# Kernel tuning notes

Measured on AMD Instinct MI355X. Metric: run time of the kernel, lower is better.

## Reference

```python
import jax, jax.numpy as jnp
import numpy as np

N = 4096      # nodes
E = 131072    # edges
C_IN = 128
HID = 128     # d_model of transformer (= embed_dim used in reshape_to_trans)
OUT = 32      # GNN output channels -> transformer seq_len
HEADS = 8
DH = HID // HEADS
FF = 2048     # torch TransformerEncoderLayer default dim_feedforward
EPS = 1e-5


def layer_norm(x, g, b):
    mu = jnp.mean(x, axis=-1, keepdims=True)
    var = jnp.mean(jnp.square(x - mu), axis=-1, keepdims=True)
    return (x - mu) * jax.lax.rsqrt(var + EPS) * g + b


def setup_inputs() -> dict:
    key = jax.random.key(0)
    ks = jax.random.split(key, 24)
    def rn(k, shape, scale=0.05):
        return jax.random.normal(k, shape, dtype=jnp.float32) * scale
    inp = {
        "x": jax.random.normal(ks[0], (N, C_IN), dtype=jnp.float32),
        "edge_index": jax.random.randint(ks[1], (2, E), 0, N, dtype=jnp.int64),
        # GCN layers
        "Wg1": rn(ks[2], (C_IN, HID)), "bg1": jnp.zeros((HID,), jnp.float32),
        "Wg2": rn(ks[3], (HID, HID)),  "bg2": jnp.zeros((HID,), jnp.float32),
        "Wg3": rn(ks[4], (HID, OUT)),  "bg3": jnp.zeros((OUT,), jnp.float32),
        # MHA
        "Wq": rn(ks[5], (HID, HID)), "bq": jnp.zeros((HID,), jnp.float32),
        "Wk": rn(ks[6], (HID, HID)), "bk": jnp.zeros((HID,), jnp.float32),
        "Wv": rn(ks[7], (HID, HID)), "bv": jnp.zeros((HID,), jnp.float32),
        "Wo": rn(ks[8], (HID, HID)), "bo": jnp.zeros((HID,), jnp.float32),
        "ln1_g": jnp.ones((HID,), jnp.float32), "ln1_b": jnp.zeros((HID,), jnp.float32),
        # FFN
        "W1": rn(ks[9], (HID, FF)),  "b1": jnp.zeros((FF,), jnp.float32),
        "W2": rn(ks[10], (FF, HID)), "b2": jnp.zeros((HID,), jnp.float32),
        "ln2_g": jnp.ones((HID,), jnp.float32), "ln2_b": jnp.zeros((HID,), jnp.float32),
    }
    return inp


def reference(x, edge_index, Wg1, bg1, Wg2, bg2, Wg3, bg3,
              Wq, bq, Wk, bk, Wv, bv, Wo, bo, ln1_g, ln1_b,
              W1, b1, W2, b2, ln2_g, ln2_b):
    # ---- GCN normalization (add self-loops, symmetric D^-1/2 (A+I) D^-1/2) ----
    loop = jnp.arange(N, dtype=edge_index.dtype)
    src = jnp.concatenate([edge_index[0], loop])
    dst = jnp.concatenate([edge_index[1], loop])
    deg = jax.ops.segment_sum(jnp.ones((E + N,), jnp.float32), dst, num_segments=N)
    dinv = jnp.where(deg > 0, jax.lax.rsqrt(deg), 0.0)
    norm = (dinv[src] * dinv[dst])[:, None]  # [E+N, 1]

    def gcn(h, W, b):
        m = h @ W                               # [N, d_out]
        agg = jax.ops.segment_sum(m[src] * norm, dst, num_segments=N)
        return agg + b

    h = jax.nn.relu(gcn(x, Wg1, bg1))
    h = jax.nn.relu(gcn(h, Wg2, bg2))
    h = jax.nn.relu(gcn(h, Wg3, bg3))           # [N, OUT]

    # ---- reshape_to_trans: [N, OUT] -> [N, OUT, HID] (repeat along embed dim) ----
    t = jnp.broadcast_to(h[:, :, None], (N, OUT, HID))

    # ---- TransformerEncoderLayer (post-norm, relu FFN, no dropout at eval) ----
    q = (t @ Wq + bq).reshape(N, OUT, HEADS, DH)
    k = (t @ Wk + bk).reshape(N, OUT, HEADS, DH)
    v = (t @ Wv + bv).reshape(N, OUT, HEADS, DH)
    scores = jnp.einsum("bqhd,bkhd->bhqk", q, k) / jnp.sqrt(jnp.float32(DH))
    attn = jax.nn.softmax(scores, axis=-1)
    ctx = jnp.einsum("bhqk,bkhd->bqhd", attn, v).reshape(N, OUT, HID)
    a = ctx @ Wo + bo
    x1 = layer_norm(t + a, ln1_g, ln1_b)
    f = jax.nn.relu(x1 @ W1 + b1) @ W2 + b2
    out = layer_norm(x1 + f, ln2_g, ln2_b)      # [N, OUT, HID]
    return out
```

## Files before the change

### kernel.cpp

```cpp
#include <hip/hip_runtime.h>

#define NN 4096
#define EE 131072
#define FFD 2048

typedef float f32x4 __attribute__((ext_vector_type(4)));
typedef __bf16 bf16x8 __attribute__((ext_vector_type(8)));
typedef unsigned int u32;
typedef u32 u32x4 __attribute__((ext_vector_type(4)));
typedef unsigned short u16;
typedef u16 u16x8 __attribute__((ext_vector_type(8)));

__device__ __forceinline__ u16 f2bf(float f) {
    unsigned u = __builtin_bit_cast(unsigned, f);
    return (u16)((u + 0x7FFFu + ((u >> 16) & 1u)) >> 16);
}
__device__ __forceinline__ float bf2f(u16 h) {
    unsigned u = ((unsigned)h) << 16;
    return __builtin_bit_cast(float, u);
}
__device__ __forceinline__ u32 cvtpk(float lo, float hi) {
    u32 r;
    asm("v_cvt_pk_bf16_f32 %0, %1, %2" : "=v"(r) : "v"(lo), "v"(hi));
    return r;
}

#define GLD16(g, l) __builtin_amdgcn_global_load_lds(                            \
    (const __attribute__((address_space(1))) void*)(g),                          \
    (__attribute__((address_space(3))) void*)(l), 16, 0, 0)

__device__ __forceinline__ int ldedge(const int* ei, int idx, int is64) {
    return is64 ? ei[2 * idx] : ei[idx];
}

__global__ void k_init(const int* __restrict__ ei, int* __restrict__ flag,
                       int* __restrict__ cnt) {
    if (blockIdx.x == 0) {
        if (threadIdx.x < 64) {
            int v = ei[2 * threadIdx.x + 1];
            unsigned long long any = __ballot(v != 0);
            if (threadIdx.x == 0) *flag = (any == 0ULL) ? 1 : 0;
        }
    } else {
        cnt[(blockIdx.x - 1) * 256 + threadIdx.x] = 0;
    }
}

__global__ void k_degi(const int* __restrict__ ei, const int* __restrict__ flag,
                       int* __restrict__ cnt) {
    int e = blockIdx.x * 256 + threadIdx.x;
    if (e >= EE) return;
    atomicAdd(&cnt[ldedge(ei, EE + e, *flag)], 1);
}
__global__ __launch_bounds__(1024) void k_scan(const int* __restrict__ cnt,
        int* __restrict__ rp, int* __restrict__ cur, float* __restrict__ dinv) {
    __shared__ int tsum[1024];
    int t = threadIdx.x;
    int c0 = cnt[t * 4], c1 = cnt[t * 4 + 1], c2 = cnt[t * 4 + 2], c3 = cnt[t * 4 + 3];
    int s = c0 + c1 + c2 + c3;
    tsum[t] = s;
    dinv[t * 4]     = rsqrtf((float)c0 + 1.0f);
    dinv[t * 4 + 1] = rsqrtf((float)c1 + 1.0f);
    dinv[t * 4 + 2] = rsqrtf((float)c2 + 1.0f);
    dinv[t * 4 + 3] = rsqrtf((float)c3 + 1.0f);
    __syncthreads();
    for (int off = 1; off < 1024; off <<= 1) {
        int v = (t >= off) ? tsum[t - off] : 0;
        __syncthreads();
        tsum[t] += v;
        __syncthreads();
    }
    int excl = tsum[t] - s;
    int p0 = excl, p1 = excl + c0, p2 = p1 + c1, p3 = p2 + c2;
    rp[t * 4] = p0; rp[t * 4 + 1] = p1; rp[t * 4 + 2] = p2; rp[t * 4 + 3] = p3;
    cur[t * 4] = p0; cur[t * 4 + 1] = p1; cur[t * 4 + 2] = p2; cur[t * 4 + 3] = p3;
    if (t == 1023) rp[4096] = excl + s;
}

__global__ __launch_bounds__(256) void k_fuse1(const int* __restrict__ ei,
        const int* __restrict__ flag, int* __restrict__ cur, int* __restrict__ es,
        const float* __restrict__ x, const float* __restrict__ Wg1,
        const float* __restrict__ dinv, float* __restrict__ ms,
        const float* __restrict__ W1, const float* __restrict__ W2,
        u16* __restrict__ w1t, u16* __restrict__ w2t,
        const float* __restrict__ Wq, const float* __restrict__ bq,
        const float* __restrict__ Wk, const float* __restrict__ bk,
        const float* __restrict__ Wv, const float* __restrict__ bv,
        const float* __restrict__ Wo, const float* __restrict__ bo,
        float* __restrict__ tc) {
    __shared__ float sm[384];
    int b = blockIdx.x, t = threadIdx.x;
    if (b < 512) {
        int e = b * 256 + t;
        int is64 = *flag;
        int s = ldedge(ei, e, is64), d = ldedge(ei, EE + e, is64);
        int pos = atomicAdd(&cur[d], 1);
        es[pos] = s;
    } else if (b < 2560) {
        int n0 = (b - 512) * 2, r = t >> 7, e = t & 127;
        sm[r * 128 + e] = x[(size_t)(n0 + r) * 128 + e];
        __syncthreads();
        float a = 0.f;
        #pragma unroll 8
        for (int c = 0; c < 128; ++c) a += sm[r * 128 + c] * Wg1[c * 128 + e];
        ms[(size_t)(n0 + r) * 128 + e] = a * dinv[n0 + r];
    } else if (b < 4608) {
        int bb = b - 2560;
        int tg = (bb & 1023) * 256 + t;
        if (bb < 1024) { int f = tg >> 7, c = tg & 127; w1t[tg] = f2bf(W1[c * 2048 + f]); }
        else           { int o = tg >> 11, f = tg & 2047; w2t[tg] = f2bf(W2[f * 128 + o]); }
    } else {
        float aq = 0, ak = 0, av = 0;
        if (t < 128) {
            for (int c = 0; c < 128; ++c) {
                aq += Wq[c * 128 + t]; ak += Wk[c * 128 + t]; av += Wv[c * 128 + t];
            }
            sm[t] = aq; sm[128 + t] = ak; sm[256 + t] = av;
            tc[t] = aq; tc[128 + t] = ak; tc[256 + t] = av;
        }
        __syncthreads();
        if (t < 128) {
            float pb = 0;
            for (int d = 0; d < 128; ++d) pb += bv[d] * Wo[d * 128 + t];
            tc[1440 + t] = pb + bo[t];
            for (int hh = 0; hh < 8; ++hh) {
                float p = 0;
                #pragma unroll
                for (int d = hh * 16; d < hh * 16 + 16; ++d) p += sm[256 + d] * Wo[d * 128 + t];
                tc[416 + hh * 128 + t] = p;
            }
        }
        if (t < 8) {
            float A = 0, B = 0, C = 0, D = 0;
            #pragma unroll
            for (int d = t * 16; d < t * 16 + 16; ++d) {
                A += sm[d] * sm[128 + d]; B += sm[d] * bk[d];
                C += bq[d] * sm[128 + d]; D += bq[d] * bk[d];
            }
            tc[384 + t] = A; tc[392 + t] = B; tc[400 + t] = C; tc[408 + t] = D;
        }
    }
}

__global__ __launch_bounds__(256) void k_gcn_mm128(const float* __restrict__ h,
        const float* __restrict__ W, const float* __restrict__ dinv, float* __restrict__ ms) {
    __shared__ float hr[2][128];
    int t = threadIdx.x, n0 = blockIdx.x * 2, r = t >> 7, e = t & 127;
    hr[r][e] = h[(size_t)(n0 + r) * 128 + e];
    __syncthreads();
    float a = 0.f;
    #pragma unroll 8
    for (int c = 0; c < 128; ++c) a += hr[r][c] * W[c * 128 + e];
    ms[(size_t)(n0 + r) * 128 + e] = a * dinv[n0 + r];
}
__global__ __launch_bounds__(256) void k_gcn_mm32(const float* __restrict__ h,
        const float* __restrict__ W, const float* __restrict__ dinv, float* __restrict__ ms) {
    __shared__ float hr[8][128];
    int t = threadIdx.x, n0 = blockIdx.x * 8;
    for (int k2 = 0; k2 < 4; ++k2) {
        int idx = k2 * 256 + t;
        hr[idx >> 7][idx & 127] = h[(size_t)n0 * 128 + idx];
    }
    __syncthreads();
    int r = t >> 5, e = t & 31;
    float a = 0.f;
    #pragma unroll 8
    for (int c = 0; c < 128; ++c) a += hr[r][c] * W[c * 32 + e];
    ms[(size_t)(n0 + r) * 32 + e] = a * dinv[n0 + r];
}

__global__ __launch_bounds__(256) void k_gath128(const int* __restrict__ es,
        const int* __restrict__ rp, const float* __restrict__ ms,
        const float* __restrict__ dinv, const float* __restrict__ b,
        float* __restrict__ hout) {
    int node = blockIdx.x * 4 + (threadIdx.x >> 6), lane = threadIdx.x & 63;
    int st = rp[node], en = rp[node + 1];
    const float2* m2 = (const float2*)ms;
    float ax0 = 0.f, ay0 = 0.f, ax1 = 0.f, ay1 = 0.f;
    int e = st;
    for (; e + 2 <= en; e += 2) {
        int s0 = es[e], s1 = es[e + 1];
        float2 v0 = m2[(size_t)s0 * 64 + lane];
        float2 v1 = m2[(size_t)s1 * 64 + lane];
        ax0 += v0.x; ay0 += v0.y; ax1 += v1.x; ay1 += v1.y;
    }
    if (e < en) {
        float2 v = m2[(size_t)es[e] * 64 + lane];
        ax0 += v.x; ay0 += v.y;
    }
    float dv = dinv[node];
    float2 self = m2[(size_t)node * 64 + lane];
    int c = lane * 2;
    hout[(size_t)node * 128 + c]     = fmaxf(dv * (ax0 + ax1 + self.x) + b[c], 0.f);
    hout[(size_t)node * 128 + c + 1] = fmaxf(dv * (ay0 + ay1 + self.y) + b[c + 1], 0.f);
}
__global__ __launch_bounds__(256) void k_gath32(const int* __restrict__ es,
        const int* __restrict__ rp, const float* __restrict__ ms,
        const float* __restrict__ dinv, const float* __restrict__ b,
        float* __restrict__ hout) {
    int node = blockIdx.x * 8 + (threadIdx.x >> 5), sl = threadIdx.x & 31;
    int st = rp[node], en = rp[node + 1];
    float a0 = 0.f, a1 = 0.f;
    int e = st;
    for (; e + 2 <= en; e += 2) {
        a0 += ms[(size_t)es[e] * 32 + sl];
        a1 += ms[(size_t)es[e + 1] * 32 + sl];
    }
    if (e < en) a0 += ms[(size_t)es[e] * 32 + sl];
    float dv = dinv[node];
    hout[(size_t)node * 32 + sl] =
        fmaxf(dv * (a0 + a1 + ms[(size_t)node * 32 + sl]) + b[sl], 0.f);
}

__global__ __launch_bounds__(256) void k_attn(const float* __restrict__ h3, const float* __restrict__ tc,
        const float* __restrict__ g1, const float* __restrict__ b1n, u16* __restrict__ x1b) {
    __shared__ float sh[32];
    __shared__ float ws_[8][32];
    int n = blockIdx.x, t = threadIdx.x;
    if (t < 32) sh[t] = h3[(size_t)n * 32 + t];
    __syncthreads();
    {
        int hh = t >> 5, i = t & 31;
        float A = tc[384 + hh], C = tc[400 + hh];
        float coef = (sh[i] * A + C) * 0.25f;
        float m = -1e30f;
        #pragma unroll
        for (int j = 0; j < 32; ++j) m = fmaxf(m, coef * sh[j]);
        float s = 0.f, wsum = 0.f;
        #pragma unroll
        for (int j = 0; j < 32; ++j) {
            float e = __expf(coef * sh[j] - m);
            s += e; wsum += e * sh[j];
        }
        ws_[hh][i] = wsum / s;
    }
    __syncthreads();
    int wave = t >> 6, lane = t & 63;
    float pb0 = tc[1440 + lane], pb1 = tc[1440 + lane + 64];
    float po0[8], po1[8];
    #pragma unroll
    for (int hh = 0; hh < 8; ++hh) {
        po0[hh] = tc[416 + hh * 128 + lane];
        po1[hh] = tc[416 + hh * 128 + lane + 64];
    }
    float ga = g1[lane], gb = g1[lane + 64], ba = b1n[lane], bb = b1n[lane + 64];
    for (int i = wave; i < 32; i += 4) {
        float y0 = sh[i] + pb0, y1 = sh[i] + pb1;
        #pragma unroll
        for (int hh = 0; hh < 8; ++hh) {
            float w = ws_[hh][i];
            y0 += w * po0[hh]; y1 += w * po1[hh];
        }
        float s1 = y0 + y1, s2 = y0 * y0 + y1 * y1;
        #pragma unroll
        for (int off = 1; off < 64; off <<= 1) {
            s1 += __shfl_xor(s1, off); s2 += __shfl_xor(s2, off);
        }
        float mu = s1 * (1.f / 128.f);
        float var = s2 * (1.f / 128.f) - mu * mu;
        float rs = rsqrtf(var + 1e-5f);
        size_t base = ((size_t)n * 32 + i) * 128;
        x1b[base + lane]      = f2bf((y0 - mu) * rs * ga + ba);
        x1b[base + lane + 64] = f2bf((y1 - mu) * rs * gb + bb);
    }
}


#define STAGE32(buf, Fb) {                                                       \
    char* db_ = (char*)(buf);                                                    \
    _Pragma("unroll") for (int c1_ = 0; c1_ < 2; ++c1_) {                        \
        int f_ = c1_ * 16 + (t >> 4);                                            \
        int bo_ = ((t & 15) * 16) ^ ((f_ & 7) << 4);                             \
        GLD16(w1t + (size_t)((Fb) + f_) * 128 + (bo_ >> 1),                      \
              db_ + c1_ * 4096 + wave * 1024);                                   \
    }                                                                            \
    _Pragma("unroll") for (int c2_ = 0; c2_ < 2; ++c2_) {                        \
        int op_ = c2_ * 32 + wave * 8 + ((t >> 3) & 7);                          \
        int pb_ = (t & 7) ^ ((t >> 3) & 7);                                      \
        int o_  = op_ * 2 + (pb_ >> 2);                                          \
        GLD16(w2t + (size_t)o_ * 2048 + (Fb) + (pb_ & 3) * 8,                    \
              db_ + 8192 + c2_ * 4096 + wave * 1024);                            \
    } }

#define FCOMP32(buf, Fb) {                                                       \
    const char* wb_ = (const char*)(buf);                                        \
    bf16x8 w2f_[8];                                                              \
    _Pragma("unroll") for (int c2_ = 0; c2_ < 8; ++c2_)                          \
        w2f_[c2_] = *(const bf16x8*)(wb_ + 8192 + (c2_ * 8 + (li >> 1)) * 128 +  \
            ((((li & 1) * 64) + g * 16) ^ ((li >> 1) << 4)));                    \
    _Pragma("unroll") for (int cf_ = 0; cf_ < 2; ++cf_) {                        \
        bf16x8 w1f_[4];                                                          \
        _Pragma("unroll") for (int ks_ = 0; ks_ < 4; ++ks_)                      \
            w1f_[ks_] = *(const bf16x8*)(wb_ + (cf_ * 16 + li) * 256 +           \
                ((ks_ * 64 + g * 16) ^ ((li & 7) << 4)));                        \
        f32x4 a0_ = (f32x4){0.f, 0.f, 0.f, 0.f};                                 \
        f32x4 a1_ = (f32x4){0.f, 0.f, 0.f, 0.f};                                 \
        _Pragma("unroll") for (int ks_ = 0; ks_ < 4; ++ks_) {                    \
            a0_ = __builtin_amdgcn_mfma_f32_16x16x32_bf16(af[0][ks_], w1f_[ks_], a0_, 0, 0, 0); \
            a1_ = __builtin_amdgcn_mfma_f32_16x16x32_bf16(af[1][ks_], w1f_[ks_], a1_, 0, 0, 0); \
        }                                                                        \
        float4 bb_;                                                              \
        bb_.x = b1[(Fb) + cf_ * 16 + li];                                        \
        u32 pkA0 = cvtpk(fmaxf(a0_[0] + bb_.x, 0.f), fmaxf(a0_[1] + bb_.x, 0.f)); \
        u32 pkA1 = cvtpk(fmaxf(a0_[2] + bb_.x, 0.f), fmaxf(a0_[3] + bb_.x, 0.f)); \
        u32 pkB0 = cvtpk(fmaxf(a1_[0] + bb_.x, 0.f), fmaxf(a1_[1] + bb_.x, 0.f)); \
        u32 pkB1 = cvtpk(fmaxf(a1_[2] + bb_.x, 0.f), fmaxf(a1_[3] + bb_.x, 0.f)); \
        int rp0_ = g * 2, rp1_ = g * 2 + 1;                                      \
        int wl_ = (cf_ * 16 + li) * 2;                                           \
        *(u16*)(hwb + rp0_ * 128 + ((wl_) ^ (rp0_ << 4)))        = (u16)pkA0;    \
        *(u16*)(hwb + rp0_ * 128 + ((64 + wl_) ^ (rp0_ << 4)))   = (u16)(pkA0 >> 16); \
        *(u16*)(hwb + rp1_ * 128 + ((wl_) ^ (rp1_ << 4)))        = (u16)pkA1;    \
        *(u16*)(hwb + rp1_ * 128 + ((64 + wl_) ^ (rp1_ << 4)))   = (u16)(pkA1 >> 16); \
        *(u16*)(hwb + (8 + rp0_) * 128 + ((wl_) ^ (rp0_ << 4)))      = (u16)pkB0; \
        *(u16*)(hwb + (8 + rp0_) * 128 + ((64 + wl_) ^ (rp0_ << 4))) = (u16)(pkB0 >> 16); \
        *(u16*)(hwb + (8 + rp1_) * 128 + ((wl_) ^ (rp1_ << 4)))      = (u16)pkB1; \
        *(u16*)(hwb + (8 + rp1_) * 128 + ((64 + wl_) ^ (rp1_ << 4))) = (u16)(pkB1 >> 16); \
    }                                                                            \
    {                                                                            \
        bf16x8 a2_[2];                                                           \
        _Pragma("unroll") for (int rf_ = 0; rf_ < 2; ++rf_)                      \
            a2_[rf_] = *(const bf16x8*)(hwb + (rf_ * 8 + (li >> 1)) * 128 +      \
                ((((li & 1) * 64) + g * 16) ^ ((li >> 1) << 4)));                \
        _Pragma("unroll") for (int c2_ = 0; c2_ < 8; ++c2_) {                    \
            acc2[0][c2_] = __builtin_amdgcn_mfma_f32_16x16x32_bf16(a2_[0], w2f_[c2_], acc2[0][c2_], 0, 0, 0); \
            acc2[1][c2_] = __builtin_amdgcn_mfma_f32_16x16x32_bf16(a2_[1], w2f_[c2_], acc2[1][c2_], 0, 0, 0); \
        }                                                                        \
    } }

__global__ __launch_bounds__(256, 3) void k_ffn(const u16* __restrict__ x1b,
        const u16* __restrict__ w1t, const u16* __restrict__ w2t,
        const float* __restrict__ b1, const float* __restrict__ b2,
        const float* __restrict__ g2, const float* __restrict__ bt2, float* __restrict__ out) {
    __shared__ u16 wA[8192];
    __shared__ u16 wB[8192];
    __shared__ u16 hid[4][1024];
    int t = threadIdx.x, wave = t >> 6, lane = t & 63;
    int g = lane >> 4, li = lane & 15;
    size_t rowbase = (size_t)blockIdx.x * 128;
    char* hwb = (char*)&hid[wave][0];

    STAGE32(wA, 0);

    bf16x8 af[2][4];
    #pragma unroll
    for (int rf = 0; rf < 2; ++rf)
    #pragma unroll
    for (int ks = 0; ks < 4; ++ks)
        af[rf][ks] = *(const bf16x8*)(x1b +
            (rowbase + wave * 32 + rf * 16 + li) * 128 + ks * 32 + g * 8);

    f32x4 acc2[2][8];
    #pragma unroll
    for (int a = 0; a < 2; ++a)
    #pragma unroll
    for (int b = 0; b < 8; ++b) acc2[a][b] = (f32x4){0.f, 0.f, 0.f, 0.f};

    __syncthreads();

    for (int F = 0; F < FFD; F += 64) {
        STAGE32(wB, F + 32);
        FCOMP32(wA, F);
        __syncthreads();
        if (F + 64 < FFD) STAGE32(wA, F + 64);
        FCOMP32(wB, F + 32);
        __syncthreads();
    }

    #pragma unroll
    for (int rf = 0; rf < 2; ++rf)
    #pragma unroll
    for (int r = 0; r < 4; ++r) {
        int lrow = wave * 32 + rf * 16 + g * 4 + r;
        size_t grow = rowbase + lrow;
        float vals[8], s1 = 0.f, s2 = 0.f;
        #pragma unroll
        for (int cf2 = 0; cf2 < 8; ++cf2) {
            int col = cf2 * 16 + li;
            float xv = bf2f(x1b[grow * 128 + col]);
            float y = xv + acc2[rf][cf2][r] + b2[col];
            vals[cf2] = y; s1 += y; s2 += y * y;
        }
        #pragma unroll
        for (int m = 1; m < 16; m <<= 1) {
            s1 += __shfl_xor(s1, m); s2 += __shfl_xor(s2, m);
        }
        float mu = s1 * (1.f / 128.f);
        float var = s2 * (1.f / 128.f) - mu * mu;
        float rs = rsqrtf(var + 1e-5f);
        #pragma unroll
        for (int cf2 = 0; cf2 < 8; ++cf2) {
            int col = cf2 * 16 + li;
            out[grow * 128 + col] = (vals[cf2] - mu) * rs * g2[col] + bt2[col];
        }
    }
}

extern "C" void kernel_launch(void* const* d_in, const int* in_sizes, int n_in,
                              void* d_out, int out_size, void* d_ws, size_t ws_size,
                              hipStream_t stream) {
    const float* x   = (const float*)d_in[0];
    const int*   ei  = (const int*)d_in[1];
    const float *Wg1 = (const float*)d_in[2],  *bg1 = (const float*)d_in[3];
    const float *Wg2 = (const float*)d_in[4],  *bg2 = (const float*)d_in[5];
    const float *Wg3 = (const float*)d_in[6],  *bg3 = (const float*)d_in[7];
    const float *Wq  = (const float*)d_in[8],  *bq  = (const float*)d_in[9];
    const float *Wk  = (const float*)d_in[10], *bk  = (const float*)d_in[11];
    const float *Wv  = (const float*)d_in[12], *bv  = (const float*)d_in[13];
    const float *Wo  = (const float*)d_in[14], *bo  = (const float*)d_in[15];
    const float *g1  = (const float*)d_in[16], *b1n = (const float*)d_in[17];
    const float *W1  = (const float*)d_in[18], *b1  = (const float*)d_in[19];
    const float *W2  = (const float*)d_in[20], *b2  = (const float*)d_in[21];
    const float *g2  = (const float*)d_in[22], *bt2 = (const float*)d_in[23];

    char* ws = (char*)d_ws;
    int*   flag = (int*)(ws + 0);
    int*   cnt  = (int*)(ws + 4096);
    int*   rp   = (int*)(ws + 20480);
    int*   cur  = (int*)(ws + 40960);
    float* dinv = (float*)(ws + 57344);
    float* ms   = (float*)(ws + 73728);
    int*   es   = (int*)(ws + 2170880);
    float* hA   = (float*)(ws + 2695168);
    float* hB   = (float*)(ws + 4792320);
    float* tc   = (float*)(ws + 6889472);
    u16*   w1t  = (u16*)(ws + 6897664);
    u16*   w2t  = (u16*)(ws + 7421952);
    u16*   x1b  = (u16*)(ws + 8388608);
    float* out  = (float*)d_out;

    k_init<<<17, 256, 0, stream>>>(ei, flag, cnt);
    k_degi<<<512, 256, 0, stream>>>(ei, flag, cnt);
    k_scan<<<1, 1024, 0, stream>>>(cnt, rp, cur, dinv);

    k_fuse1<<<4609, 256, 0, stream>>>(ei, flag, cur, es, x, Wg1, dinv, ms,
                                      W1, W2, w1t, w2t,
                                      Wq, bq, Wk, bk, Wv, bv, Wo, bo, tc);

    k_gath128<<<1024, 256, 0, stream>>>(es, rp, ms, dinv, bg1, hA);
    k_gcn_mm128<<<2048, 256, 0, stream>>>(hA, Wg2, dinv, ms);
    k_gath128<<<1024, 256, 0, stream>>>(es, rp, ms, dinv, bg2, hB);
    k_gcn_mm32<<<512, 256, 0, stream>>>(hB, Wg3, dinv, ms);
    k_gath32<<<512, 256, 0, stream>>>(es, rp, ms, dinv, bg3, hA);

    k_attn<<<4096, 256, 0, stream>>>(hA, tc, g1, b1n, x1b);

    k_ffn<<<1024, 256, 0, stream>>>(x1b, w1t, w2t, b1, b2, g2, bt2, out);
}
```

Before: 288.0 us.

## Fuse layer-3 gather into attention kernel and tile weight transposes through LDS

The final GCN gather (32 channels) is merged into the attention/LayerNorm kernel, which now handles two nodes per block, so h3 no longer round-trips through global memory and one launch is removed. The W1/W2 bf16 transposes move from one element per thread with strided uncoalesced reads to 64x64 tiles staged in padded shared memory, so both reads and writes are coalesced. This enlarges k_fuse1's shared memory for every block and puts the serial gather on only 64 threads ahead of the attention work in each block.

```diff
diff --git a/kernel.cpp b/kernel.cpp
--- a/kernel.cpp
+++ b/kernel.cpp
@@ -88,7 +88,7 @@
         const float* __restrict__ Wv, const float* __restrict__ bv,
         const float* __restrict__ Wo, const float* __restrict__ bo,
         float* __restrict__ tc) {
-    __shared__ float sm[384];
+    __shared__ float smem[64 * 65];
     int b = blockIdx.x, t = threadIdx.x;
     if (b < 512) {
         int e = b * 256 + t;
@@ -98,24 +98,49 @@
         es[pos] = s;
     } else if (b < 2560) {
         int n0 = (b - 512) * 2, r = t >> 7, e = t & 127;
-        sm[r * 128 + e] = x[(size_t)(n0 + r) * 128 + e];
+        smem[r * 128 + e] = x[(size_t)(n0 + r) * 128 + e];
         __syncthreads();
         float a = 0.f;
         #pragma unroll 8
-        for (int c = 0; c < 128; ++c) a += sm[r * 128 + c] * Wg1[c * 128 + e];
+        for (int c = 0; c < 128; ++c) a += smem[r * 128 + c] * Wg1[c * 128 + e];
         ms[(size_t)(n0 + r) * 128 + e] = a * dinv[n0 + r];
-    } else if (b < 4608) {
+    } else if (b < 2624) {
         int bb = b - 2560;
-        int tg = (bb & 1023) * 256 + t;
-        if (bb < 1024) { int f = tg >> 7, c = tg & 127; w1t[tg] = f2bf(W1[c * 2048 + f]); }
-        else           { int o = tg >> 11, f = tg & 2047; w2t[tg] = f2bf(W2[f * 128 + o]); }
+        int c0 = (bb >> 5) * 64, f0 = (bb & 31) * 64;
+        int rr = t >> 6, col = t & 63;
+        #pragma unroll
+        for (int k = 0; k < 16; ++k) {
+            int row = k * 4 + rr;
+            smem[row * 65 + col] = W1[(size_t)(c0 + row) * 2048 + f0 + col];
+        }
+        __syncthreads();
+        #pragma unroll
+        for (int k = 0; k < 16; ++k) {
+            int frow = k * 4 + rr;
+            w1t[(size_t)(f0 + frow) * 128 + c0 + col] = f2bf(smem[col * 65 + frow]);
+        }
+    } else if (b < 2688) {
+        int bb = b - 2624;
+        int f0 = (bb >> 1) * 64, o0 = (bb & 1) * 64;
+        int rr = t >> 6, col = t & 63;
+        #pragma unroll
+        for (int k = 0; k < 16; ++k) {
+            int row = k * 4 + rr;
+            smem[row * 65 + col] = W2[(size_t)(f0 + row) * 128 + o0 + col];
+        }
+        __syncthreads();
+        #pragma unroll
+        for (int k = 0; k < 16; ++k) {
+            int orow = k * 4 + rr;
+            w2t[(size_t)(o0 + orow) * 2048 + f0 + col] = f2bf(smem[col * 65 + orow]);
+        }
     } else {
         float aq = 0, ak = 0, av = 0;
         if (t < 128) {
             for (int c = 0; c < 128; ++c) {
                 aq += Wq[c * 128 + t]; ak += Wk[c * 128 + t]; av += Wv[c * 128 + t];
             }
-            sm[t] = aq; sm[128 + t] = ak; sm[256 + t] = av;
+            smem[t] = aq; smem[128 + t] = ak; smem[256 + t] = av;
             tc[t] = aq; tc[128 + t] = ak; tc[256 + t] = av;
         }
         __syncthreads();
@@ -126,7 +151,7 @@
             for (int hh = 0; hh < 8; ++hh) {
                 float p = 0;
                 #pragma unroll
-                for (int d = hh * 16; d < hh * 16 + 16; ++d) p += sm[256 + d] * Wo[d * 128 + t];
+                for (int d = hh * 16; d < hh * 16 + 16; ++d) p += smem[256 + d] * Wo[d * 128 + t];
                 tc[416 + hh * 128 + t] = p;
             }
         }
@@ -134,8 +159,8 @@
             float A = 0, B = 0, C = 0, D = 0;
             #pragma unroll
             for (int d = t * 16; d < t * 16 + 16; ++d) {
-                A += sm[d] * sm[128 + d]; B += sm[d] * bk[d];
-                C += bq[d] * sm[128 + d]; D += bq[d] * bk[d];
+                A += smem[d] * smem[128 + d]; B += smem[d] * bk[d];
+                C += bq[d] * smem[128 + d];   D += bq[d] * bk[d];
             }
             tc[384 + t] = A; tc[392 + t] = B; tc[400 + t] = C; tc[408 + t] = D;
         }
@@ -194,48 +219,51 @@
     hout[(size_t)node * 128 + c]     = fmaxf(dv * (ax0 + ax1 + self.x) + b[c], 0.f);
     hout[(size_t)node * 128 + c + 1] = fmaxf(dv * (ay0 + ay1 + self.y) + b[c + 1], 0.f);
 }
-__global__ __launch_bounds__(256) void k_gath32(const int* __restrict__ es,
+
+__global__ __launch_bounds__(256) void k_ga(const int* __restrict__ es,
         const int* __restrict__ rp, const float* __restrict__ ms,
-        const float* __restrict__ dinv, const float* __restrict__ b,
-        float* __restrict__ hout) {
-    int node = blockIdx.x * 8 + (threadIdx.x >> 5), sl = threadIdx.x & 31;
-    int st = rp[node], en = rp[node + 1];
-    float a0 = 0.f, a1 = 0.f;
-    int e = st;
-    for (; e + 2 <= en; e += 2) {
-        a0 += ms[(size_t)es[e] * 32 + sl];
-        a1 += ms[(size_t)es[e + 1] * 32 + sl];
-    }
-    if (e < en) a0 += ms[(size_t)es[e] * 32 + sl];
-    float dv = dinv[node];
-    hout[(size_t)node * 32 + sl] =
-        fmaxf(dv * (a0 + a1 + ms[(size_t)node * 32 + sl]) + b[sl], 0.f);
-}
-
-__global__ __launch_bounds__(256) void k_attn(const float* __restrict__ h3, const float* __restrict__ tc,
-        const float* __restrict__ g1, const float* __restrict__ b1n, u16* __restrict__ x1b) {
-    __shared__ float sh[32];
-    __shared__ float ws_[8][32];
-    int n = blockIdx.x, t = threadIdx.x;
-    if (t < 32) sh[t] = h3[(size_t)n * 32 + t];
-    __syncthreads();
-    {
-        int hh = t >> 5, i = t & 31;
+        const float* __restrict__ dinv, const float* __restrict__ bg3,
+        const float* __restrict__ tc, const float* __restrict__ g1,
+        const float* __restrict__ b1n, u16* __restrict__ x1b) {
+    __shared__ float sh[2][32];
+    __shared__ float wsm[2][8][32];
+    int b = blockIdx.x, t = threadIdx.x;
+    int n0 = b * 2;
+    if (t < 64) {
+        int ni = t >> 5, sl = t & 31;
+        int node = n0 + ni;
+        int st = rp[node], en = rp[node + 1];
+        float a0 = 0.f, a1 = 0.f;
+        int e = st;
+        for (; e + 2 <= en; e += 2) {
+            a0 += ms[(size_t)es[e] * 32 + sl];
+            a1 += ms[(size_t)es[e + 1] * 32 + sl];
+        }
+        if (e < en) a0 += ms[(size_t)es[e] * 32 + sl];
+        float dv = dinv[node];
+        sh[ni][sl] = fmaxf(dv * (a0 + a1 + ms[(size_t)node * 32 + sl]) + bg3[sl], 0.f);
+    }
+    __syncthreads();
+    #pragma unroll
+    for (int rep = 0; rep < 2; ++rep) {
+        int idx = rep * 256 + t;
+        int ni = idx >> 8, hh = (idx >> 5) & 7, i = idx & 31;
         float A = tc[384 + hh], C = tc[400 + hh];
-        float coef = (sh[i] * A + C) * 0.25f;
+        float coef = (sh[ni][i] * A + C) * 0.25f;
         float m = -1e30f;
         #pragma unroll
-        for (int j = 0; j < 32; ++j) m = fmaxf(m, coef * sh[j]);
+        for (int j = 0; j < 32; ++j) m = fmaxf(m, coef * sh[ni][j]);
         float s = 0.f, wsum = 0.f;
         #pragma unroll
         for (int j = 0; j < 32; ++j) {
-            float e = __expf(coef * sh[j] - m);
-            s += e; wsum += e * sh[j];
-        }
-        ws_[hh][i] = wsum / s;
+            float e = __expf(coef * sh[ni][j] - m);
+            s += e; wsum += e * sh[ni][j];
+        }
+        wsm[ni][hh][i] = wsum / s;
     }
     __syncthreads();
     int wave = t >> 6, lane = t & 63;
+    int ni = wave >> 1;
     float pb0 = tc[1440 + lane], pb1 = tc[1440 + lane + 64];
     float po0[8], po1[8];
     #pragma unroll
@@ -244,11 +272,12 @@
         po1[hh] = tc[416 + hh * 128 + lane + 64];
     }
     float ga = g1[lane], gb = g1[lane + 64], ba = b1n[lane], bb = b1n[lane + 64];
-    for (int i = wave; i < 32; i += 4) {
-        float y0 = sh[i] + pb0, y1 = sh[i] + pb1;
+    size_t nbase = (size_t)(n0 + ni) * 32;
+    for (int i = (wave & 1); i < 32; i += 2) {
+        float y0 = sh[ni][i] + pb0, y1 = sh[ni][i] + pb1;
         #pragma unroll
         for (int hh = 0; hh < 8; ++hh) {
-            float w = ws_[hh][i];
+            float w = wsm[ni][hh][i];
             y0 += w * po0[hh]; y1 += w * po1[hh];
         }
         float s1 = y0 + y1, s2 = y0 * y0 + y1 * y1;
@@ -259,12 +288,11 @@
         float mu = s1 * (1.f / 128.f);
         float var = s2 * (1.f / 128.f) - mu * mu;
         float rs = rsqrtf(var + 1e-5f);
-        size_t base = ((size_t)n * 32 + i) * 128;
+        size_t base = (nbase + i) * 128;
         x1b[base + lane]      = f2bf((y0 - mu) * rs * ga + ba);
         x1b[base + lane + 64] = f2bf((y1 - mu) * rs * gb + bb);
     }
 }
-
 
 #define STAGE32(buf, Fb) {                                                       \
     char* db_ = (char*)(buf);                                                    \
@@ -299,12 +327,11 @@
             a0_ = __builtin_amdgcn_mfma_f32_16x16x32_bf16(af[0][ks_], w1f_[ks_], a0_, 0, 0, 0); \
             a1_ = __builtin_amdgcn_mfma_f32_16x16x32_bf16(af[1][ks_], w1f_[ks_], a1_, 0, 0, 0); \
         }                                                                        \
-        float4 bb_;                                                              \
-        bb_.x = b1[(Fb) + cf_ * 16 + li];                                        \
-        u32 pkA0 = cvtpk(fmaxf(a0_[0] + bb_.x, 0.f), fmaxf(a0_[1] + bb_.x, 0.f)); \
-        u32 pkA1 = cvtpk(fmaxf(a0_[2] + bb_.x, 0.f), fmaxf(a0_[3] + bb_.x, 0.f)); \
-        u32 pkB0 = cvtpk(fmaxf(a1_[0] + bb_.x, 0.f), fmaxf(a1_[1] + bb_.x, 0.f)); \
-        u32 pkB1 = cvtpk(fmaxf(a1_[2] + bb_.x, 0.f), fmaxf(a1_[3] + bb_.x, 0.f)); \
+        float bias_ = b1[(Fb) + cf_ * 16 + li];                                  \
+        u32 pkA0 = cvtpk(fmaxf(a0_[0] + bias_, 0.f), fmaxf(a0_[1] + bias_, 0.f)); \
+        u32 pkA1 = cvtpk(fmaxf(a0_[2] + bias_, 0.f), fmaxf(a0_[3] + bias_, 0.f)); \
+        u32 pkB0 = cvtpk(fmaxf(a1_[0] + bias_, 0.f), fmaxf(a1_[1] + bias_, 0.f)); \
+        u32 pkB1 = cvtpk(fmaxf(a1_[2] + bias_, 0.f), fmaxf(a1_[3] + bias_, 0.f)); \
         int rp0_ = g * 2, rp1_ = g * 2 + 1;                                      \
         int wl_ = (cf_ * 16 + li) * 2;                                           \
         *(u16*)(hwb + rp0_ * 128 + ((wl_) ^ (rp0_ << 4)))        = (u16)pkA0;    \
@@ -432,7 +459,7 @@
     k_degi<<<512, 256, 0, stream>>>(ei, flag, cnt);
     k_scan<<<1, 1024, 0, stream>>>(cnt, rp, cur, dinv);
 
-    k_fuse1<<<4609, 256, 0, stream>>>(ei, flag, cur, es, x, Wg1, dinv, ms,
+    k_fuse1<<<2689, 256, 0, stream>>>(ei, flag, cur, es, x, Wg1, dinv, ms,
                                       W1, W2, w1t, w2t,
                                       Wq, bq, Wk, bk, Wv, bv, Wo, bo, tc);
 
@@ -440,9 +467,8 @@
     k_gcn_mm128<<<2048, 256, 0, stream>>>(hA, Wg2, dinv, ms);
     k_gath128<<<1024, 256, 0, stream>>>(es, rp, ms, dinv, bg2, hB);
     k_gcn_mm32<<<512, 256, 0, stream>>>(hB, Wg3, dinv, ms);
-    k_gath32<<<512, 256, 0, stream>>>(es, rp, ms, dinv, bg3, hA);
-
-    k_attn<<<4096, 256, 0, stream>>>(hA, tc, g1, b1n, x1b);
+
+    k_ga<<<2048, 256, 0, stream>>>(es, rp, ms, dinv, bg3, tc, g1, b1n, x1b);
 
     k_ffn<<<1024, 256, 0, stream>>>(x1b, w1t, w2t, b1, b2, g2, bt2, out);
 }
```

After: 285.7 us. About the same (-0.8%).
